# Optimization experiments

Hardware: AMD Instinct MI355X
Metric: run time of the kernel (lower is better)

## Reference

```python
import jax, jax.numpy as jnp
import numpy as np

N_NODES = 50000
N_EDGES = 500000
HIDDEN = 128
HEADS = 8
HEAD_DIM = HIDDEN // HEADS
EPS = 1e-16  # PyG softmax denominator epsilon


def _kaiming(key, shape):
    fan_in = shape[0]
    return jax.random.normal(key, shape, dtype=jnp.float32) * np.sqrt(2.0 / fan_in)


def prelu(x, a):
    return jnp.maximum(x, 0.0) + a * jnp.minimum(x, 0.0)


def transformer_conv(x, src, dst, Wq, bq, Wk, bk, Wv, bv, Ws, bs):
    """PyG TransformerConv (concat=True, root_weight=True, beta=False), eval mode."""
    N = x.shape[0]
    q = (x @ Wq + bq).reshape(N, HEADS, HEAD_DIM)
    k = (x @ Wk + bk).reshape(N, HEADS, HEAD_DIM)
    v = (x @ Wv + bv).reshape(N, HEADS, HEAD_DIM)
    # per-edge attention: query from destination, key/value from source
    score = jnp.einsum('ehd,ehd->eh', q[dst], k[src]) / np.sqrt(HEAD_DIM)  # [E,H]
    m = jax.ops.segment_max(score, dst, num_segments=N)                     # [N,H]
    e = jnp.exp(score - m[dst])
    s = jax.ops.segment_sum(e, dst, num_segments=N)
    alpha = e / (s[dst] + EPS)                                              # [E,H]
    agg = jax.ops.segment_sum(alpha[..., None] * v[src], dst, num_segments=N)
    return agg.reshape(N, HIDDEN) + x @ Ws + bs  # skip connection (lin_skip)


def setup_inputs() -> dict:
    key = jax.random.key(0)
    ks = jax.random.split(key, 12)
    inp = {
        'x': jax.random.normal(ks[0], (N_NODES, HIDDEN), dtype=jnp.float32),
        'edge_index': jax.random.randint(ks[1], (2, N_EDGES), 0, N_NODES, dtype=jnp.int64 if jax.config.jax_enable_x64 else jnp.int32),
        'prelu_w': jnp.full((1,), 0.25, dtype=jnp.float32),
    }
    i = 2
    for layer in (1, 2):
        for nm in ('q', 'k', 'v', 's'):
            inp[f'W{nm}{layer}'] = _kaiming(ks[i], (HIDDEN, HIDDEN))
            inp[f'b{nm}{layer}'] = jnp.zeros((HIDDEN,), dtype=jnp.float32)
            i += 1
        ks = jax.random.split(ks[-1], 12)
        i = 0
    return inp


def reference(x, edge_index, prelu_w,
              Wq1, bq1, Wk1, bk1, Wv1, bv1, Ws1, bs1,
              Wq2, bq2, Wk2, bk2, Wv2, bv2, Ws2, bs2):
    src, dst = edge_index[0], edge_index[1]
    o = transformer_conv(x, src, dst, Wq1, bq1, Wk1, bk1, Wv1, bv1, Ws1, bs1)
    o = prelu(o, prelu_w)
    o = transformer_conv(o, src, dst, Wq2, bq2, Wk2, bk2, Wv2, bv2, Ws2, bs2)
    o = o + x  # residual
    return prelu(o, prelu_w)
```

## Files before the change

### kernel.cpp

```cpp
#include <hip/hip_runtime.h>

#define NN 50000
#define NE 500000
#define HID 128
#define MT4 3128
#define MT4_PER_XCD 391

typedef __attribute__((ext_vector_type(8))) short short8;
typedef __attribute__((ext_vector_type(8))) _Float16 half8;
typedef __attribute__((ext_vector_type(2))) _Float16 half2v;
typedef __attribute__((ext_vector_type(4))) float f32x4;
typedef unsigned short ushort_t;
typedef unsigned int uint32;
typedef _Float16 half_t;

__device__ __forceinline__ ushort_t f2h(float f) {
    union { half_t h; ushort_t u; } x; x.h = (half_t)f; return x.u;
}
__device__ __forceinline__ half2v u2h2(uint32 u) {
    union { uint32 u; half2v h; } x; x.u = u; return x.h;
}

__global__ void pack_w2(const float* __restrict__ Wq1, const float* __restrict__ Wk1,
                        const float* __restrict__ Wv1, const float* __restrict__ Ws1,
                        const float* __restrict__ Wq2, const float* __restrict__ Wk2,
                        const float* __restrict__ Wv2, const float* __restrict__ Ws2,
                        ushort_t* __restrict__ Bt1, ushort_t* __restrict__ Bt2)
{
    int idx = blockIdx.x * 256 + threadIdx.x;
    int layer = idx >> 16;
    int r = idx & 65535;
    int col = r >> 7;
    int kk = r & 127;
    int wsel = col >> 7;
    const float* W = (layer == 0)
        ? ((wsel == 0) ? Wq1 : (wsel == 1) ? Wk1 : (wsel == 2) ? Wv1 : Ws1)
        : ((wsel == 0) ? Wq2 : (wsel == 1) ? Wk2 : (wsel == 2) ? Wv2 : Ws2);
    float val = W[kk * HID + (col & 127)];
    if (wsel == 0) val *= 0.25f;
    (layer == 0 ? Bt1 : Bt2)[r] = f2h(val);
}

template <int LAYER>
__global__ __launch_bounds__(256) void gemm_mfma(
    const float* __restrict__ Xf, const ushort_t* __restrict__ Xh,
    const ushort_t* __restrict__ Bt,
    const float* __restrict__ bqp, const float* __restrict__ bkp,
    const float* __restrict__ bvp, const float* __restrict__ bsp,
    ushort_t* __restrict__ Qb, ushort_t* __restrict__ KVb, ushort_t* __restrict__ Sfb)
{
    __shared__ ushort_t As[64 * 128];
    __shared__ ushort_t Bs[128 * 128];
    const int wgid = blockIdx.x;
    const int xcd = wgid & 7, kidx = wgid >> 3;
    const int local = xcd * MT4_PER_XCD + kidx;
    const int mtile = local >> 2;
    const int g = local & 3;
    const int Mbase = mtile * 64;
    const int tid = threadIdx.x;
    const int lane = tid & 63, wave = tid >> 6;

    #pragma unroll
    for (int it = 0; it < 4; ++it) {
        int lin = it * 256 + tid;
        int row = lin >> 4, s = lin & 15;
        int rg = Mbase + row; if (rg >= NN) rg = NN - 1;
        short8 v;
        if (LAYER == 1) {
            float4 f0 = *reinterpret_cast<const float4*>(Xf + (size_t)rg * HID + s * 8);
            float4 f1 = *reinterpret_cast<const float4*>(Xf + (size_t)rg * HID + s * 8 + 4);
            v[0] = (short)f2h(f0.x); v[1] = (short)f2h(f0.y);
            v[2] = (short)f2h(f0.z); v[3] = (short)f2h(f0.w);
            v[4] = (short)f2h(f1.x); v[5] = (short)f2h(f1.y);
            v[6] = (short)f2h(f1.z); v[7] = (short)f2h(f1.w);
        } else {
            v = *reinterpret_cast<const short8*>(Xh + (size_t)rg * HID + s * 8);
        }
        *reinterpret_cast<short8*>((char*)As + row * 256 + ((s * 16) ^ ((row & 7) * 16))) = v;
    }
    #pragma unroll
    for (int it = 0; it < 8; ++it) {
        int lin = it * 256 + tid;
        int col = lin >> 4, s = lin & 15;
        short8 v = *reinterpret_cast<const short8*>(
            Bt + (size_t)(g * 128 + col) * HID + s * 8);
        *reinterpret_cast<short8*>((char*)Bs + col * 256 + ((s * 16) ^ ((col & 7) * 16))) = v;
    }
    __syncthreads();

    const int l15 = lane & 15;
    const int wrow = wave * 16;
    f32x4 acc[8] = {};
    #pragma unroll
    for (int kk = 0; kk < 4; ++kk) {
        int kbyte = kk * 64 + (lane >> 4) * 16;
        int ar = wrow + l15;
        half8 a = *reinterpret_cast<const half8*>(
            (const char*)As + ar * 256 + (kbyte ^ ((ar & 7) * 16)));
        #pragma unroll
        for (int nb = 0; nb < 8; ++nb) {
            int c = nb * 16 + l15;
            half8 b = *reinterpret_cast<const half8*>(
                (const char*)Bs + c * 256 + (kbyte ^ ((c & 7) * 16)));
            acc[nb] = __builtin_amdgcn_mfma_f32_16x16x32_f16(a, b, acc[nb], 0, 0, 0);
        }
    }
    __syncthreads();

    const float* bias = (g == 0) ? bqp : (g == 1) ? bkp : (g == 2) ? bvp : bsp;
    float* Cs = reinterpret_cast<float*>(Bs);
    #pragma unroll
    for (int nb = 0; nb < 8; ++nb) {
        int c = nb * 16 + l15;
        float bb = bias[c];
        if (g == 0) bb *= 0.25f;
        #pragma unroll
        for (int r = 0; r < 4; ++r) {
            int rl = wrow + (lane >> 4) * 4 + r;
            Cs[rl * 128 + c] = acc[nb][r] + bb;
        }
    }
    __syncthreads();

    #pragma unroll
    for (int it = 0; it < 4; ++it) {
        int lin = it * 256 + tid;
        int row = lin >> 4, s = lin & 15;
        int rg = Mbase + row;
        if (rg < NN) {
            float4 v0 = *reinterpret_cast<float4*>(&Cs[row * 128 + s * 8]);
            float4 v1 = *reinterpret_cast<float4*>(&Cs[row * 128 + s * 8 + 4]);
            short8 o;
            o[0] = (short)f2h(v0.x); o[1] = (short)f2h(v0.y);
            o[2] = (short)f2h(v0.z); o[3] = (short)f2h(v0.w);
            o[4] = (short)f2h(v1.x); o[5] = (short)f2h(v1.y);
            o[6] = (short)f2h(v1.z); o[7] = (short)f2h(v1.w);
            ushort_t* dst = (g == 0) ? (Qb  + (size_t)rg * HID + s * 8)
                          : (g == 1) ? (KVb + (size_t)rg * 256 + s * 8)
                          : (g == 2) ? (KVb + (size_t)rg * 256 + 128 + s * 8)
                          :            (Sfb + (size_t)rg * HID + s * 8);
            *reinterpret_cast<short8*>(dst) = o;
        }
    }
}

__global__ void hist_kernel(const int* __restrict__ dst, int* __restrict__ counts)
{
    int e = blockIdx.x * blockDim.x + threadIdx.x;
    if (e < NE) atomicAdd(&counts[dst[e]], 1);
}

#define SCAN_B 196

__global__ __launch_bounds__(256) void block_sums(const int* __restrict__ counts,
                                                  int* __restrict__ bsum)
{
    int i = blockIdx.x * 256 + threadIdx.x;
    int v = (i < NN) ? counts[i] : 0;
    #pragma unroll
    for (int o = 1; o < 64; o <<= 1) v += __shfl_xor(v, o);
    __shared__ int ws[4];
    if ((threadIdx.x & 63) == 0) ws[threadIdx.x >> 6] = v;
    __syncthreads();
    if (threadIdx.x == 0) bsum[blockIdx.x] = ws[0] + ws[1] + ws[2] + ws[3];
}

__global__ __launch_bounds__(256) void scan_bsums(const int* __restrict__ bsum,
                                                  int* __restrict__ bbase)
{
    __shared__ int sh[256];
    int t = threadIdx.x;
    int v = (t < SCAN_B) ? bsum[t] : 0;
    sh[t] = v;
    __syncthreads();
    for (int o = 1; o < 256; o <<= 1) {
        int u = (t >= o) ? sh[t - o] : 0;
        __syncthreads();
        sh[t] += u;
        __syncthreads();
    }
    bbase[t] = (t > 0) ? sh[t - 1] : 0;
}

__global__ __launch_bounds__(256) void write_offsets(const int* __restrict__ counts,
        const int* __restrict__ bbase, int* __restrict__ offsets, int* __restrict__ cursor)
{
    __shared__ int sh[256];
    int t = threadIdx.x;
    int i = blockIdx.x * 256 + t;
    int v = (i < NN) ? counts[i] : 0;
    sh[t] = v;
    __syncthreads();
    for (int o = 1; o < 256; o <<= 1) {
        int u = (t >= o) ? sh[t - o] : 0;
        __syncthreads();
        sh[t] += u;
        __syncthreads();
    }
    int excl = sh[t] - v + bbase[blockIdx.x];
    if (i < NN) { offsets[i] = excl; cursor[i] = excl; }
    if (i == NN - 1) offsets[NN] = excl + v;
}

__global__ void scatter_kernel(const int* __restrict__ src, const int* __restrict__ dst,
                               int* __restrict__ cursor, int* __restrict__ csr_src)
{
    int e = blockIdx.x * blockDim.x + threadIdx.x;
    if (e < NE) {
        int pos = atomicAdd(&cursor[dst[e]], 1);
        csr_src[pos] = src[e];
    }
}

template <int LAYER>
__global__ __launch_bounds__(256) void edge_aggregate(
    const half_t* __restrict__ Qh, const half_t* __restrict__ KVh,
    const half_t* __restrict__ Sh,
    const int* __restrict__ offsets, const int* __restrict__ csr_src,
    const float* __restrict__ xres, const float* __restrict__ prelu_w,
    float* __restrict__ outF, ushort_t* __restrict__ outH)
{
    const int lane = threadIdx.x & 63;
    const int wid  = __builtin_amdgcn_readfirstlane((int)(threadIdx.x >> 6));
    const int node = blockIdx.x * 4 + wid;
    const bool hi  = lane >= 32;
    const int  c   = lane & 31;

    uint2 qu = *reinterpret_cast<const uint2*>(Qh + (size_t)node * HID + c * 4);
    half2v qa = u2h2(qu.x), qb = u2h2(qu.y);
    const float q0 = (float)qa[0], q1 = (float)qa[1];
    const float q2 = (float)qb[0], q3 = (float)qb[1];

    const int beg = offsets[node];
    const int end = offsets[node + 1];

    float den = 0.f, a0 = 0.f, a1 = 0.f, a2 = 0.f, a3 = 0.f;

#define COMPUTE(KU, VU) {                                                      \
        half2v k01 = u2h2((KU).x), k23 = u2h2((KU).y);                         \
        float p = (float)k01[0] * q0 + (float)k01[1] * q1                      \
                + (float)k23[0] * q2 + (float)k23[1] * q3;                     \
        p += __shfl_xor(p, 1); p += __shfl_xor(p, 2);                          \
        float w = __expf(p);                                                   \
        den += w;                                                              \
        half2v v01 = u2h2((VU).x), v23 = u2h2((VU).y);                         \
        a0 += w * (float)v01[0]; a1 += w * (float)v01[1];                      \
        a2 += w * (float)v23[0]; a3 += w * (float)v23[1]; }

    int i = beg;
    for (; i + 8 <= end; i += 8) {
        uint2 ku[4], vu[4];
        #pragma unroll
        for (int j = 0; j < 4; ++j) {
            int s = hi ? csr_src[i + 2 * j + 1] : csr_src[i + 2 * j];
            const half_t* kv = KVh + (size_t)s * 256 + c * 4;
            ku[j] = *reinterpret_cast<const uint2*>(kv);
            vu[j] = *reinterpret_cast<const uint2*>(kv + 128);
        }
        #pragma unroll
        for (int j = 0; j < 4; ++j) COMPUTE(ku[j], vu[j])
    }
    for (; i + 2 <= end; i += 2) {
        int s = hi ? csr_src[i + 1] : csr_src[i];
        const half_t* kv = KVh + (size_t)s * 256 + c * 4;
        uint2 ku = *reinterpret_cast<const uint2*>(kv);
        uint2 vu = *reinterpret_cast<const uint2*>(kv + 128);
        COMPUTE(ku, vu)
    }
    if (i < end) {
        int s = csr_src[i];
        const half_t* kv = KVh + (size_t)s * 256 + c * 4;
        uint2 ku = *reinterpret_cast<const uint2*>(kv);
        uint2 vu = *reinterpret_cast<const uint2*>(kv + 128);
        half2v k01 = u2h2(ku.x), k23 = u2h2(ku.y);
        float p = (float)k01[0] * q0 + (float)k01[1] * q1
                + (float)k23[0] * q2 + (float)k23[1] * q3;
        p += __shfl_xor(p, 1); p += __shfl_xor(p, 2);
        float w = hi ? 0.f : __expf(p);
        den += w;
        half2v v01 = u2h2(vu.x), v23 = u2h2(vu.y);
        a0 += w * (float)v01[0]; a1 += w * (float)v01[1];
        a2 += w * (float)v23[0]; a3 += w * (float)v23[1];
    }
#undef COMPUTE

    den += __shfl_xor(den, 32);
    a0 += __shfl_xor(a0, 32); a1 += __shfl_xor(a1, 32);
    a2 += __shfl_xor(a2, 32); a3 += __shfl_xor(a3, 32);

    if (!hi) {
        float inv = (den > 0.f) ? 1.f / den : 0.f;
        uint2 su = *reinterpret_cast<const uint2*>(Sh + (size_t)node * HID + c * 4);
        half2v s01 = u2h2(su.x), s23 = u2h2(su.y);
        float r0 = a0 * inv + (float)s01[0];
        float r1 = a1 * inv + (float)s01[1];
        float r2 = a2 * inv + (float)s23[0];
        float r3 = a3 * inv + (float)s23[1];
        if (LAYER == 2) {
            float4 xr = *reinterpret_cast<const float4*>(xres + (size_t)node * HID + c * 4);
            r0 += xr.x; r1 += xr.y; r2 += xr.z; r3 += xr.w;
        }
        const float al = prelu_w[0];
        r0 = fmaxf(r0, 0.f) + al * fminf(r0, 0.f);
        r1 = fmaxf(r1, 0.f) + al * fminf(r1, 0.f);
        r2 = fmaxf(r2, 0.f) + al * fminf(r2, 0.f);
        r3 = fmaxf(r3, 0.f) + al * fminf(r3, 0.f);
        if (LAYER == 1) {
            uint2 o;
            o.x = (uint32)f2h(r0) | ((uint32)f2h(r1) << 16);
            o.y = (uint32)f2h(r2) | ((uint32)f2h(r3) << 16);
            *reinterpret_cast<uint2*>(outH + (size_t)node * HID + c * 4) = o;
        } else {
            float4 o; o.x = r0; o.y = r1; o.z = r2; o.w = r3;
            *reinterpret_cast<float4*>(outF + (size_t)node * HID + c * 4) = o;
        }
    }
}

extern "C" void kernel_launch(void* const* d_in, const int* in_sizes, int n_in,
                              void* d_out, int out_size, void* d_ws, size_t ws_size,
                              hipStream_t stream)
{
    const float* x       = (const float*)d_in[0];
    const int*   ei      = (const int*)d_in[1];
    const float* prelu_w = (const float*)d_in[2];
    const float* Wq1 = (const float*)d_in[3],  *bq1 = (const float*)d_in[4];
    const float* Wk1 = (const float*)d_in[5],  *bk1 = (const float*)d_in[6];
    const float* Wv1 = (const float*)d_in[7],  *bv1 = (const float*)d_in[8];
    const float* Ws1 = (const float*)d_in[9],  *bs1 = (const float*)d_in[10];
    const float* Wq2 = (const float*)d_in[11], *bq2 = (const float*)d_in[12];
    const float* Wk2 = (const float*)d_in[13], *bk2 = (const float*)d_in[14];
    const float* Wv2 = (const float*)d_in[15], *bv2 = (const float*)d_in[16];
    const float* Ws2 = (const float*)d_in[17], *bs2 = (const float*)d_in[18];

    char* w = (char*)d_ws;
    size_t off = 0;
    auto alloc = [&](size_t bytes) { void* p = w + off; off += (bytes + 255) & ~(size_t)255; return p; };
    ushort_t* x1h  = (ushort_t*)alloc((size_t)NN * HID * 2);
    ushort_t* Qb   = (ushort_t*)alloc((size_t)NN * HID * 2);
    ushort_t* KVb  = (ushort_t*)alloc((size_t)NN * 256 * 2);
    ushort_t* Sfb  = (ushort_t*)alloc((size_t)NN * HID * 2);
    ushort_t* Bt1  = (ushort_t*)alloc((size_t)512 * 128 * 2);
    ushort_t* Bt2  = (ushort_t*)alloc((size_t)512 * 128 * 2);
    int* counts  = (int*)alloc(NN * sizeof(int));
    int* bsum    = (int*)alloc(256 * sizeof(int));
    int* bbase   = (int*)alloc(256 * sizeof(int));
    int* offsets = (int*)alloc((NN + 1) * sizeof(int));
    int* cursor  = (int*)alloc(NN * sizeof(int));
    int* csr_src = (int*)alloc(NE * sizeof(int));
    (void)ws_size; (void)in_sizes; (void)n_in; (void)out_size;

    const int* srcIdx = ei;
    const int* dstIdx = ei + NE;

    hipMemsetAsync(counts, 0, NN * sizeof(int), stream);
    hist_kernel<<<(NE + 255) / 256, 256, 0, stream>>>(dstIdx, counts);
    block_sums<<<SCAN_B, 256, 0, stream>>>(counts, bsum);
    scan_bsums<<<1, 256, 0, stream>>>(bsum, bbase);
    write_offsets<<<SCAN_B, 256, 0, stream>>>(counts, bbase, offsets, cursor);
    scatter_kernel<<<(NE + 255) / 256, 256, 0, stream>>>(srcIdx, dstIdx, cursor, csr_src);

    pack_w2<<<512, 256, 0, stream>>>(Wq1, Wk1, Wv1, Ws1, Wq2, Wk2, Wv2, Ws2, Bt1, Bt2);

    gemm_mfma<1><<<MT4, 256, 0, stream>>>(x, nullptr, Bt1, bq1, bk1, bv1, bs1,
                                          Qb, KVb, Sfb);
    edge_aggregate<1><<<NN / 4, 256, 0, stream>>>((const half_t*)Qb, (const half_t*)KVb,
                                                  (const half_t*)Sfb, offsets, csr_src,
                                                  nullptr, prelu_w, nullptr, x1h);
    gemm_mfma<2><<<MT4, 256, 0, stream>>>(nullptr, x1h, Bt2, bq2, bk2, bv2, bs2,
                                          Qb, KVb, Sfb);
    edge_aggregate<2><<<NN / 4, 256, 0, stream>>>((const half_t*)Qb, (const half_t*)KVb,
                                                  (const half_t*)Sfb, offsets, csr_src,
                                                  x, prelu_w, (float*)d_out, nullptr);
}
```

Measured before the change: 205.5 us.

## Fuse CSR build, histogram and weight packing into fewer launches with grid barriers

Cuts the launch count from eleven to six. The memset, weight packing and counts-zeroing are merged into one prep kernel, and the degree histogram rides as extra blocks on the first GEMM launch. The block-sum, scan, offset and scatter kernels become one persistent 256-block kernel with software grid barriers. This removes launch gaps and small-kernel tails, but the spin barriers assume all 256 blocks are co-resident.

```diff
diff --git a/kernel.cpp b/kernel.cpp
--- a/kernel.cpp
+++ b/kernel.cpp
@@ -5,6 +5,9 @@
 #define HID 128
 #define MT4 3128
 #define MT4_PER_XCD 391
+#define HISTB 1954
+#define SCAN_B 196
+#define CSRB 256
 
 typedef __attribute__((ext_vector_type(8))) short short8;
 typedef __attribute__((ext_vector_type(8))) _Float16 half8;
@@ -21,37 +24,45 @@
     union { uint32 u; half2v h; } x; x.u = u; return x.h;
 }
 
-__global__ void pack_w2(const float* __restrict__ Wq1, const float* __restrict__ Wk1,
-                        const float* __restrict__ Wv1, const float* __restrict__ Ws1,
-                        const float* __restrict__ Wq2, const float* __restrict__ Wk2,
-                        const float* __restrict__ Wv2, const float* __restrict__ Ws2,
-                        ushort_t* __restrict__ Bt1, ushort_t* __restrict__ Bt2)
-{
-    int idx = blockIdx.x * 256 + threadIdx.x;
-    int layer = idx >> 16;
-    int r = idx & 65535;
-    int col = r >> 7;
-    int kk = r & 127;
-    int wsel = col >> 7;
-    const float* W = (layer == 0)
-        ? ((wsel == 0) ? Wq1 : (wsel == 1) ? Wk1 : (wsel == 2) ? Wv1 : Ws1)
-        : ((wsel == 0) ? Wq2 : (wsel == 1) ? Wk2 : (wsel == 2) ? Wv2 : Ws2);
-    float val = W[kk * HID + (col & 127)];
-    if (wsel == 0) val *= 0.25f;
-    (layer == 0 ? Bt1 : Bt2)[r] = f2h(val);
+__global__ __launch_bounds__(256) void prep(
+    const float* __restrict__ Wq1, const float* __restrict__ Wk1,
+    const float* __restrict__ Wv1, const float* __restrict__ Ws1,
+    const float* __restrict__ Wq2, const float* __restrict__ Wk2,
+    const float* __restrict__ Wv2, const float* __restrict__ Ws2,
+    ushort_t* __restrict__ Bt1, ushort_t* __restrict__ Bt2,
+    int* __restrict__ counts, int* __restrict__ bars)
+{
+    int b = blockIdx.x, t = threadIdx.x;
+    if (b < 512) {
+        int idx = b * 256 + t;
+        int layer = idx >> 16;
+        int r = idx & 65535;
+        int col = r >> 7;
+        int kk = r & 127;
+        int wsel = col >> 7;
+        const float* W = (layer == 0)
+            ? ((wsel == 0) ? Wq1 : (wsel == 1) ? Wk1 : (wsel == 2) ? Wv1 : Ws1)
+            : ((wsel == 0) ? Wq2 : (wsel == 1) ? Wk2 : (wsel == 2) ? Wv2 : Ws2);
+        float val = W[kk * HID + (col & 127)];
+        if (wsel == 0) val *= 0.25f;
+        (layer == 0 ? Bt1 : Bt2)[r] = f2h(val);
+    } else if (b < 512 + SCAN_B) {
+        int i = (b - 512) * 256 + t;
+        if (i < NN) counts[i] = 0;
+    } else {
+        if (t < 8) bars[t] = 0;
+    }
 }
 
 template <int LAYER>
-__global__ __launch_bounds__(256) void gemm_mfma(
+__device__ __forceinline__ void gemm_body(
+    ushort_t* As, ushort_t* Bs, int wgid,
     const float* __restrict__ Xf, const ushort_t* __restrict__ Xh,
     const ushort_t* __restrict__ Bt,
     const float* __restrict__ bqp, const float* __restrict__ bkp,
     const float* __restrict__ bvp, const float* __restrict__ bsp,
     ushort_t* __restrict__ Qb, ushort_t* __restrict__ KVb, ushort_t* __restrict__ Sfb)
 {
-    __shared__ ushort_t As[64 * 128];
-    __shared__ ushort_t Bs[128 * 128];
-    const int wgid = blockIdx.x;
     const int xcd = wgid & 7, kidx = wgid >> 3;
     const int local = xcd * MT4_PER_XCD + kidx;
     const int mtile = local >> 2;
@@ -144,69 +155,102 @@
     }
 }
 
-__global__ void hist_kernel(const int* __restrict__ dst, int* __restrict__ counts)
-{
-    int e = blockIdx.x * blockDim.x + threadIdx.x;
-    if (e < NE) atomicAdd(&counts[dst[e]], 1);
-}
-
-#define SCAN_B 196
-
-__global__ __launch_bounds__(256) void block_sums(const int* __restrict__ counts,
-                                                  int* __restrict__ bsum)
-{
-    int i = blockIdx.x * 256 + threadIdx.x;
-    int v = (i < NN) ? counts[i] : 0;
-    #pragma unroll
-    for (int o = 1; o < 64; o <<= 1) v += __shfl_xor(v, o);
+__global__ __launch_bounds__(256) void gemm1_hist(
+    const float* __restrict__ Xf, const ushort_t* __restrict__ Bt,
+    const float* __restrict__ bqp, const float* __restrict__ bkp,
+    const float* __restrict__ bvp, const float* __restrict__ bsp,
+    ushort_t* __restrict__ Qb, ushort_t* __restrict__ KVb, ushort_t* __restrict__ Sfb,
+    const int* __restrict__ dstIdx, int* __restrict__ counts)
+{
+    __shared__ ushort_t As[64 * 128];
+    __shared__ ushort_t Bs[128 * 128];
+    if (blockIdx.x < MT4) {
+        gemm_body<1>(As, Bs, blockIdx.x, Xf, nullptr, Bt,
+                     bqp, bkp, bvp, bsp, Qb, KVb, Sfb);
+    } else {
+        int e = (blockIdx.x - MT4) * 256 + threadIdx.x;
+        if (e < NE) atomicAdd(&counts[dstIdx[e]], 1);
+    }
+}
+
+__global__ __launch_bounds__(256) void gemm2(
+    const ushort_t* __restrict__ Xh, const ushort_t* __restrict__ Bt,
+    const float* __restrict__ bqp, const float* __restrict__ bkp,
+    const float* __restrict__ bvp, const float* __restrict__ bsp,
+    ushort_t* __restrict__ Qb, ushort_t* __restrict__ KVb, ushort_t* __restrict__ Sfb)
+{
+    __shared__ ushort_t As[64 * 128];
+    __shared__ ushort_t Bs[128 * 128];
+    gemm_body<2>(As, Bs, blockIdx.x, nullptr, Xh, Bt,
+                 bqp, bkp, bvp, bsp, Qb, KVb, Sfb);
+}
+
+__device__ __forceinline__ void grid_barrier(int* ctr)
+{
+    __syncthreads();
+    if (threadIdx.x == 0) {
+        __threadfence();
+        atomicAdd(ctr, 1);
+        while (__hip_atomic_load(ctr, __ATOMIC_RELAXED, __HIP_MEMORY_SCOPE_AGENT) < CSRB)
+            __builtin_amdgcn_s_sleep(2);
+        __threadfence();
+    }
+    __syncthreads();
+}
+
+__global__ __launch_bounds__(256) void csr_build(
+    const int* __restrict__ src, const int* __restrict__ dst,
+    const int* __restrict__ counts, int* __restrict__ bsum, int* __restrict__ bbase,
+    int* __restrict__ offsets, int* __restrict__ cursor, int* __restrict__ csr_src,
+    int* __restrict__ bars)
+{
+    __shared__ int sh[256];
     __shared__ int ws[4];
-    if ((threadIdx.x & 63) == 0) ws[threadIdx.x >> 6] = v;
-    __syncthreads();
-    if (threadIdx.x == 0) bsum[blockIdx.x] = ws[0] + ws[1] + ws[2] + ws[3];
-}
-
-__global__ __launch_bounds__(256) void scan_bsums(const int* __restrict__ bsum,
-                                                  int* __restrict__ bbase)
-{
-    __shared__ int sh[256];
-    int t = threadIdx.x;
-    int v = (t < SCAN_B) ? bsum[t] : 0;
-    sh[t] = v;
-    __syncthreads();
-    for (int o = 1; o < 256; o <<= 1) {
-        int u = (t >= o) ? sh[t - o] : 0;
+    const int t = threadIdx.x, b = blockIdx.x;
+
+    if (b < SCAN_B) {
+        int i = b * 256 + t;
+        int v = (i < NN) ? counts[i] : 0;
+        #pragma unroll
+        for (int o = 1; o < 64; o <<= 1) v += __shfl_xor(v, o);
+        if ((t & 63) == 0) ws[t >> 6] = v;
         __syncthreads();
-        sh[t] += u;
+        if (t == 0) bsum[b] = ws[0] + ws[1] + ws[2] + ws[3];
+    }
+    grid_barrier(bars + 0);
+
+    if (b == 0) {
+        int v = (t < SCAN_B) ? bsum[t] : 0;
+        sh[t] = v;
         __syncthreads();
-    }
-    bbase[t] = (t > 0) ? sh[t - 1] : 0;
-}
-
-__global__ __launch_bounds__(256) void write_offsets(const int* __restrict__ counts,
-        const int* __restrict__ bbase, int* __restrict__ offsets, int* __restrict__ cursor)
-{
-    __shared__ int sh[256];
-    int t = threadIdx.x;
-    int i = blockIdx.x * 256 + t;
-    int v = (i < NN) ? counts[i] : 0;
-    sh[t] = v;
-    __syncthreads();
-    for (int o = 1; o < 256; o <<= 1) {
-        int u = (t >= o) ? sh[t - o] : 0;
+        for (int o = 1; o < 256; o <<= 1) {
+            int u = (t >= o) ? sh[t - o] : 0;
+            __syncthreads();
+            sh[t] += u;
+            __syncthreads();
+        }
+        if (t < SCAN_B) bbase[t] = (t > 0) ? sh[t - 1] : 0;
+    }
+    grid_barrier(bars + 1);
+
+    if (b < SCAN_B) {
+        int i = b * 256 + t;
+        int v = (i < NN) ? counts[i] : 0;
+        sh[t] = v;
         __syncthreads();
-        sh[t] += u;
-        __syncthreads();
-    }
-    int excl = sh[t] - v + bbase[blockIdx.x];
-    if (i < NN) { offsets[i] = excl; cursor[i] = excl; }
-    if (i == NN - 1) offsets[NN] = excl + v;
-}
-
-__global__ void scatter_kernel(const int* __restrict__ src, const int* __restrict__ dst,
-                               int* __restrict__ cursor, int* __restrict__ csr_src)
-{
-    int e = blockIdx.x * blockDim.x + threadIdx.x;
-    if (e < NE) {
+        for (int o = 1; o < 256; o <<= 1) {
+            int u = (t >= o) ? sh[t - o] : 0;
+            __syncthreads();
+            sh[t] += u;
+            __syncthreads();
+        }
+        int excl = sh[t] - v + bbase[b];
+        if (i < NN) { offsets[i] = excl; cursor[i] = excl; }
+        if (i == NN - 1) offsets[NN] = excl + v;
+    }
+    grid_barrier(bars + 2);
+
+    for (int e = b * 256 + t; e < NE; e += CSRB * 256) {
         int pos = atomicAdd(&cursor[dst[e]], 1);
         csr_src[pos] = src[e];
     }
@@ -348,27 +392,23 @@
     int* offsets = (int*)alloc((NN + 1) * sizeof(int));
     int* cursor  = (int*)alloc(NN * sizeof(int));
     int* csr_src = (int*)alloc(NE * sizeof(int));
+    int* bars    = (int*)alloc(8 * sizeof(int));
     (void)ws_size; (void)in_sizes; (void)n_in; (void)out_size;
 
     const int* srcIdx = ei;
     const int* dstIdx = ei + NE;
 
-    hipMemsetAsync(counts, 0, NN * sizeof(int), stream);
-    hist_kernel<<<(NE + 255) / 256, 256, 0, stream>>>(dstIdx, counts);
-    block_sums<<<SCAN_B, 256, 0, stream>>>(counts, bsum);
-    scan_bsums<<<1, 256, 0, stream>>>(bsum, bbase);
-    write_offsets<<<SCAN_B, 256, 0, stream>>>(counts, bbase, offsets, cursor);
-    scatter_kernel<<<(NE + 255) / 256, 256, 0, stream>>>(srcIdx, dstIdx, cursor, csr_src);
-
-    pack_w2<<<512, 256, 0, stream>>>(Wq1, Wk1, Wv1, Ws1, Wq2, Wk2, Wv2, Ws2, Bt1, Bt2);
-
-    gemm_mfma<1><<<MT4, 256, 0, stream>>>(x, nullptr, Bt1, bq1, bk1, bv1, bs1,
-                                          Qb, KVb, Sfb);
+    prep<<<512 + SCAN_B + 1, 256, 0, stream>>>(Wq1, Wk1, Wv1, Ws1,
+                                               Wq2, Wk2, Wv2, Ws2,
+                                               Bt1, Bt2, counts, bars);
+    gemm1_hist<<<MT4 + HISTB, 256, 0, stream>>>(x, Bt1, bq1, bk1, bv1, bs1,
+                                                Qb, KVb, Sfb, dstIdx, counts);
+    csr_build<<<CSRB, 256, 0, stream>>>(srcIdx, dstIdx, counts, bsum, bbase,
+                                        offsets, cursor, csr_src, bars);
     edge_aggregate<1><<<NN / 4, 256, 0, stream>>>((const half_t*)Qb, (const half_t*)KVb,
                                                   (const half_t*)Sfb, offsets, csr_src,
                                                   nullptr, prelu_w, nullptr, x1h);
-    gemm_mfma<2><<<MT4, 256, 0, stream>>>(nullptr, x1h, Bt2, bq2, bk2, bv2, bs2,
-                                          Qb, KVb, Sfb);
+    gemm2<<<MT4, 256, 0, stream>>>(x1h, Bt2, bq2, bk2, bv2, bs2, Qb, KVb, Sfb);
     edge_aggregate<2><<<NN / 4, 256, 0, stream>>>((const half_t*)Qb, (const half_t*)KVb,
                                                   (const half_t*)Sfb, offsets, csr_src,
                                                   x, prelu_w, (float*)d_out, nullptr);
```

After: 240.9 us. 1.17x slower.
